# Kernel tuning notes

Measured on AMD Instinct MI355X. Metric: run time of the kernel, lower is better.

## Reference

```python
import jax, jax.numpy as jnp
import numpy as np


def _dct_basis_64() -> jnp.ndarray:
    """8x8 2D DCT-II basis as a conv filter of shape [8, 8, 1, 64] (HWIO).

    Filter k = 8*u + v is the (u, v) DCT basis function:
      alpha(u)*alpha(v)*cos((2x+1)u pi/16)*cos((2y+1)v pi/16)
    """
    N = 8
    xs = np.arange(N)
    # 1D DCT matrix: C[u, x]
    C = np.cos((2 * xs[None, :] + 1) * xs[:, None] * np.pi / (2 * N))
    alpha = np.full(N, np.sqrt(2.0 / N))
    alpha[0] = np.sqrt(1.0 / N)
    C = alpha[:, None] * C  # [u, x]
    # basis[x, y, u, v] = C[u, x] * C[v, y]
    basis = np.einsum('ux,vy->xyuv', C, C).reshape(N, N, 1, N * N)
    return jnp.asarray(basis, dtype=jnp.float32)


def setup_inputs() -> dict:
    key = jax.random.key(0)
    inputs = jax.random.normal(key, (16, 256, 256, 1), dtype=jnp.float32)
    dct_basis = _dct_basis_64()  # [8, 8, 1, 64]
    return {"inputs": inputs, "dct_basis": dct_basis}


def reference(inputs, dct_basis):
    # Block DCT: stride-8 SAME conv -> [B, 32, 32, 64]
    x = jax.lax.conv_general_dilated(
        inputs, dct_basis,
        window_strides=(8, 8), padding='SAME',
        dimension_numbers=('NHWC', 'HWIO', 'NHWC'))
    gamma = 1000000.0
    bins = jnp.arange(-60, 61, dtype=x.dtype)  # 121 thresholds
    # Soft CDF at every threshold in one vectorized pass:
    # [B, 121, Hc, Wc, 64] -> sum over spatial -> [B, 121, 64]
    s = jax.nn.sigmoid(gamma * (x[:, None] - bins[None, :, None, None, None]))
    x4 = jnp.sum(s, axis=(2, 3)) / 1024.0
    # Differentiate adjacent soft-CDF values -> 120-bin soft histogram
    x5 = x4[:, 0:120, :] - x4[:, 1:121, :]
    return x5[..., None]  # [B, 120, 64, 1]
```

## Files before the change

### kernel.cpp

```cpp
#include <hip/hip_runtime.h>
#include <math.h>


__global__ __launch_bounds__(64) void dct_hist_kernel(
    const float* __restrict__ in,
    const float* __restrict__ basis,
    float* __restrict__ out)
{
    __shared__ float tvs[16 * 73];
    __shared__ float coef[64 * 17];

    const int t  = threadIdx.x;
    const int wg = blockIdx.x;
    const int b  = wg >> 6;
    const int g  = wg & 63;
    const int by = g >> 1;
    const int bx0 = (g & 1) * 16;

    const int i = t >> 2;
    const int h = t & 3;

    const float SQRT8 = 2.8284271247461903f;

    float Cm[8][8];
    #pragma unroll
    for (int a = 0; a < 8; ++a)
        #pragma unroll
        for (int x = 0; x < 8; ++x)
            Cm[a][x] = basis[x * 512 + a * 8] * SQRT8;

    const float* p0 = in + ((b * 256 + by * 8) * 256 + (bx0 + i) * 8);
    #pragma unroll
    for (int xl = 0; xl < 2; ++xl) {
        const int x = 2 * h + xl;
        const float4 r0 = *(const float4*)(p0 + x * 256);
        const float4 r1 = *(const float4*)(p0 + x * 256 + 4);
        const float p[8] = {r0.x, r0.y, r0.z, r0.w, r1.x, r1.y, r1.z, r1.w};
        #pragma unroll
        for (int v = 0; v < 8; ++v) {
            float s = 0.0f;
            #pragma unroll
            for (int y = 0; y < 8; ++y) s = fmaf(Cm[v][y], p[y], s);
            tvs[i * 73 + x * 9 + v] = s;
        }
    }

    float Cu0[8], Cu1[8];
    #pragma unroll
    for (int x = 0; x < 8; ++x) {
        Cu0[x] = basis[x * 512 + (2 * h) * 8] * SQRT8;
        Cu1[x] = basis[x * 512 + (2 * h + 1) * 8] * SQRT8;
    }

    __syncthreads();

    #pragma unroll
    for (int v = 0; v < 8; ++v) {
        float tcol[8];
        #pragma unroll
        for (int x = 0; x < 8; ++x) tcol[x] = tvs[i * 73 + x * 9 + v];
        float xv0 = 0.0f, xv1 = 0.0f;
        #pragma unroll
        for (int x = 0; x < 8; ++x) {
            xv0 = fmaf(Cu0[x], tcol[x], xv0);
            xv1 = fmaf(Cu1[x], tcol[x], xv1);
        }
        coef[((2 * h) * 8 + v) * 17 + i] = xv0;
        coef[((2 * h + 1) * 8 + v) * 17 + i] = xv1;
    }

    __syncthreads();

    unsigned h0 = 0, h1 = 0, h2 = 0, h3 = 0, h4 = 0, h5 = 0;
    float* outb = out + b * (120 * 64);
    const float EPS = 3e-5f;

    #pragma unroll
    for (int blk = 0; blk < 16; ++blk) {
        const float xv = coef[t * 17 + blk];
        const int j = (int)floorf(xv + 60.0f);
        if (j >= -1 && j <= 120) {
            const float bf  = (float)j - 60.0f;
            const float dlo = xv - bf;
            const float dhi = xv - (bf + 1.0f);
            if (dlo > EPS && dhi < -EPS) {
                const unsigned w = (unsigned)(j - 48);
                if (w < 24u) {
                    const unsigned inc = 1u << (8 * (w & 3));
                    const unsigned sel = w >> 2;
                    h0 += (sel == 0) ? inc : 0u;
                    h1 += (sel == 1) ? inc : 0u;
                    h2 += (sel == 2) ? inc : 0u;
                    h3 += (sel == 3) ? inc : 0u;
                    h4 += (sel == 4) ? inc : 0u;
                    h5 += (sel == 5) ? inc : 0u;
                } else if (j >= 0 && j <= 119) {
                    atomicAdd(&outb[j * 64 + t], 1.0f / 1024.0f);
                }
            } else {
                const float slo = 1.0f / (1.0f + expf(-1e6f * dlo));
                const float shi = 1.0f / (1.0f + expf(-1e6f * dhi));
                if (j >= 0 && j <= 119)
                    atomicAdd(&outb[j * 64 + t], (slo - shi) * (1.0f / 1024.0f));
                if (j - 1 >= 0)
                    atomicAdd(&outb[(j - 1) * 64 + t], (1.0f - slo) * (1.0f / 1024.0f));
                if (j + 1 <= 119)
                    atomicAdd(&outb[(j + 1) * 64 + t], shi * (1.0f / 1024.0f));
            }
        }
    }

    const unsigned hw[6] = {h0, h1, h2, h3, h4, h5};
    #pragma unroll
    for (int w = 0; w < 24; ++w) {
        const float cnt = (float)((hw[w >> 2] >> (8 * (w & 3))) & 255u);
        if (cnt != 0.0f)
            atomicAdd(&outb[(48 + w) * 64 + t], cnt * (1.0f / 1024.0f));
    }
}

extern "C" void kernel_launch(void* const* d_in, const int* in_sizes, int n_in,
                              void* d_out, int out_size, void* d_ws, size_t ws_size,
                              hipStream_t stream) {
    const float* inputs = (const float*)d_in[0];
    const float* basis  = (const float*)d_in[1];
    float* out = (float*)d_out;

    (void)hipMemsetAsync(out, 0, (size_t)out_size * sizeof(float), stream);

    dct_hist_kernel<<<dim3(1024), dim3(64), 0, stream>>>(inputs, basis, out);
}
```

Measured before the change: 64.77 us.

## Halve blocks per workgroup to 8 and launch twice as many workgroups

```diff
diff --git a/kernel.cpp b/kernel.cpp
--- a/kernel.cpp
+++ b/kernel.cpp
@@ -7,18 +7,18 @@
     const float* __restrict__ basis,
     float* __restrict__ out)
 {
-    __shared__ float tvs[16 * 73];
-    __shared__ float coef[64 * 17];
+    __shared__ float tvs[576];
+    __shared__ float coef[576];
 
     const int t  = threadIdx.x;
     const int wg = blockIdx.x;
-    const int b  = wg >> 6;
-    const int g  = wg & 63;
-    const int by = g >> 1;
-    const int bx0 = (g & 1) * 16;
+    const int b  = wg >> 7;
+    const int g  = wg & 127;
+    const int by = g >> 2;
+    const int bx0 = (g & 3) * 8;
 
-    const int i = t >> 2;
-    const int h = t & 3;
+    const int i = t & 7;
+    const int h = t >> 3;
 
     const float SQRT8 = 2.8284271247461903f;
 
@@ -29,44 +29,34 @@
         for (int x = 0; x < 8; ++x)
             Cm[a][x] = basis[x * 512 + a * 8] * SQRT8;
 
-    const float* p0 = in + ((b * 256 + by * 8) * 256 + (bx0 + i) * 8);
+    float Cu[8];
     #pragma unroll
-    for (int xl = 0; xl < 2; ++xl) {
-        const int x = 2 * h + xl;
-        const float4 r0 = *(const float4*)(p0 + x * 256);
-        const float4 r1 = *(const float4*)(p0 + x * 256 + 4);
+    for (int x = 0; x < 8; ++x)
+        Cu[x] = basis[x * 512 + h * 8] * SQRT8;
+
+    const float* p0 = in + ((b * 256 + by * 8 + h) * 256 + (bx0 + i) * 8);
+    {
+        const float4 r0 = *(const float4*)(p0);
+        const float4 r1 = *(const float4*)(p0 + 4);
         const float p[8] = {r0.x, r0.y, r0.z, r0.w, r1.x, r1.y, r1.z, r1.w};
         #pragma unroll
         for (int v = 0; v < 8; ++v) {
             float s = 0.0f;
             #pragma unroll
             for (int y = 0; y < 8; ++y) s = fmaf(Cm[v][y], p[y], s);
-            tvs[i * 73 + x * 9 + v] = s;
+            tvs[(8 * h + v) * 9 + i] = s;
         }
-    }
-
-    float Cu0[8], Cu1[8];
-    #pragma unroll
-    for (int x = 0; x < 8; ++x) {
-        Cu0[x] = basis[x * 512 + (2 * h) * 8] * SQRT8;
-        Cu1[x] = basis[x * 512 + (2 * h + 1) * 8] * SQRT8;
     }
 
     __syncthreads();
 
     #pragma unroll
     for (int v = 0; v < 8; ++v) {
-        float tcol[8];
+        float xv = 0.0f;
         #pragma unroll
-        for (int x = 0; x < 8; ++x) tcol[x] = tvs[i * 73 + x * 9 + v];
-        float xv0 = 0.0f, xv1 = 0.0f;
-        #pragma unroll
-        for (int x = 0; x < 8; ++x) {
-            xv0 = fmaf(Cu0[x], tcol[x], xv0);
-            xv1 = fmaf(Cu1[x], tcol[x], xv1);
-        }
-        coef[((2 * h) * 8 + v) * 17 + i] = xv0;
-        coef[((2 * h + 1) * 8 + v) * 17 + i] = xv1;
+        for (int x = 0; x < 8; ++x)
+            xv = fmaf(Cu[x], tvs[(8 * x + v) * 9 + i], xv);
+        coef[(8 * h + v) * 9 + i] = xv;
     }
 
     __syncthreads();
@@ -76,8 +66,8 @@
     const float EPS = 3e-5f;
 
     #pragma unroll
-    for (int blk = 0; blk < 16; ++blk) {
-        const float xv = coef[t * 17 + blk];
+    for (int blk = 0; blk < 8; ++blk) {
+        const float xv = coef[t * 9 + blk];
         const int j = (int)floorf(xv + 60.0f);
         if (j >= -1 && j <= 120) {
             const float bf  = (float)j - 60.0f;
@@ -128,5 +118,5 @@
 
     (void)hipMemsetAsync(out, 0, (size_t)out_size * sizeof(float), stream);
 
-    dct_hist_kernel<<<dim3(1024), dim3(64), 0, stream>>>(inputs, basis, out);
+    dct_hist_kernel<<<dim3(2048), dim3(64), 0, stream>>>(inputs, basis, out);
 }
```

Result: slower. 66.63 us (+2.9%).
